# Kernel tuning notes

Measured on AMD Instinct MI355X. Metric: run time of the kernel, lower is better.

The kernel has to match this reference:

```python
import jax, jax.numpy as jnp
import numpy as np

MODEL_DIM = 1024
NUM_HEADS = 16
K_DIM = MODEL_DIM // NUM_HEADS


def setup_inputs() -> dict:
    key = jax.random.key(0)
    k1, k2, k3 = jax.random.split(key, 3)
    x = jax.random.normal(k1, (4, 2048, MODEL_DIM), dtype=jnp.float32)
    # nn.Linear(model_dim, 3*model_dim, bias=False): store as [D, 3D] so y = x @ W
    wqkv = jax.random.normal(k2, (MODEL_DIM, 3 * MODEL_DIM), dtype=jnp.float32) * (MODEL_DIM ** -0.5)
    wo = jax.random.normal(k3, (MODEL_DIM, MODEL_DIM), dtype=jnp.float32) * (MODEL_DIM ** -0.5)
    return {"x": x, "wqkv": wqkv, "wo": wo}


def reference(x, wqkv, wo):
    B, L, D = x.shape
    H, K = NUM_HEADS, K_DIM
    qkv = jnp.einsum("bld,de->ble", x, wqkv)  # [B, L, 3D]
    q, k, v = jnp.split(qkv, 3, axis=-1)
    # Faithful to source: plain reshape (no transpose) into [B, H, L, K]
    qh = q.reshape(B, H, L, K)
    kh = k.reshape(B, H, L, K)
    vh = v.reshape(B, H, L, K)
    scores = jnp.einsum("bhlk,bhmk->bhlm", qh, kh) / jnp.sqrt(jnp.float32(K))
    # Faithful quirk: softmax over dim=1 (head axis), as in the source
    probs = jax.nn.softmax(scores, axis=1)
    attended = jnp.einsum("bhlm,bhmk->bhlk", probs, vh)  # [B, H, L, K]
    concatted = attended.transpose(0, 2, 1, 3).reshape(B, L, D)
    return jnp.einsum("bld,de->ble", concatted, wo)
```

## Files before the change

### kernel.cpp

```cpp
#include <hip/hip_runtime.h>
#include <hip/hip_bf16.h>
#include <stdint.h>

typedef __attribute__((ext_vector_type(8))) short short8;
typedef __attribute__((ext_vector_type(4))) float floatx4;

#define QSCALE 0.18033688f

__device__ __forceinline__ unsigned short f2bf(float f) {
    unsigned int u = __float_as_uint(f);
    u += 0x7fffu + ((u >> 16) & 1u);
    return (unsigned short)(u >> 16);
}
__device__ __forceinline__ unsigned int pack2bf(float a, float b) {
    __hip_bfloat162 h = __float22bfloat162_rn(make_float2(a, b));
    return *reinterpret_cast<unsigned int*>(&h);
}

__device__ __forceinline__ void async16(const void* g, void* l) {
    __builtin_amdgcn_global_load_lds(
        (const __attribute__((address_space(1))) unsigned int*)g,
        (__attribute__((address_space(3))) unsigned int*)l, 16, 0, 0);
}

__global__ __launch_bounds__(256) void cvt_bf16(const float* __restrict__ src,
                                                unsigned short* __restrict__ dst, int n8) {
    int i = blockIdx.x * 256 + threadIdx.x;
    if (i >= n8) return;
    const float4 a = ((const float4*)src)[2 * i];
    const float4 b = ((const float4*)src)[2 * i + 1];
    ushort4 lo, hi;
    lo.x = f2bf(a.x); lo.y = f2bf(a.y); lo.z = f2bf(a.z); lo.w = f2bf(a.w);
    hi.x = f2bf(b.x); hi.y = f2bf(b.y); hi.z = f2bf(b.z); hi.w = f2bf(b.w);
    ((ushort4*)dst)[2 * i] = lo;
    ((ushort4*)dst)[2 * i + 1] = hi;
}

__global__ __launch_bounds__(256) void tcvt(const float* __restrict__ src,
                                            unsigned short* __restrict__ dst, int R, int C) {
    __shared__ unsigned short t[64][72];
    const int tid = threadIdx.x;
    const int r0 = blockIdx.y * 64, c0 = blockIdx.x * 64;
    #pragma unroll
    for (int it = 0; it < 4; it++) {
        int idx = it * 256 + tid;
        int rr = idx >> 4, cc = (idx & 15) * 4;
        float4 v = *(const float4*)(src + (size_t)(r0 + rr) * C + c0 + cc);
        t[cc + 0][rr] = f2bf(v.x);
        t[cc + 1][rr] = f2bf(v.y);
        t[cc + 2][rr] = f2bf(v.z);
        t[cc + 3][rr] = f2bf(v.w);
    }
    __syncthreads();
    #pragma unroll
    for (int it = 0; it < 2; it++) {
        int idx = it * 256 + tid;
        int cc = idx >> 3, r8 = (idx & 7) * 8;
        short8 v = *(const short8*)&t[cc][r8];
        *(short8*)(dst + (size_t)(c0 + cc) * R + r0 + r8) = v;
    }
}

__global__ __launch_bounds__(256) void vtrans(const unsigned short* __restrict__ vb,
                                              unsigned short* __restrict__ vbt) {
    __shared__ unsigned short t[64][72];
    const int tid = threadIdx.x;
    const int bh = blockIdx.y, m0 = blockIdx.x * 64;
    const unsigned short* src = vb + ((size_t)bh * 2048 + m0) * 64;
    unsigned short* dst = vbt + ((size_t)bh << 17) + m0;
    union { short8 v; unsigned short u[8]; } tmp;
    #pragma unroll
    for (int it = 0; it < 2; it++) {
        int idx = it * 256 + tid;
        int m = idx >> 3, c8 = (idx & 7) * 8;
        tmp.v = *(const short8*)(src + (size_t)m * 64 + c8);
        #pragma unroll
        for (int j = 0; j < 8; j++) t[c8 + j][m] = tmp.u[j];
    }
    __syncthreads();
    #pragma unroll
    for (int it = 0; it < 2; it++) {
        int idx = it * 256 + tid;
        int k = idx >> 3, c8 = (idx & 7) * 8;
        short8 v = *(const short8*)&t[k][c8];
        *(short8*)(dst + (size_t)k * 2048 + c8) = v;
    }
}

__global__ __launch_bounds__(256) void qkv_gemm(
    const unsigned short* __restrict__ A, const unsigned short* __restrict__ Bt,
    unsigned short* __restrict__ qb, unsigned short* __restrict__ kb,
    unsigned short* __restrict__ vb)
{
    __shared__ __align__(16) unsigned short Smem[2 * 128 * 32];
    unsigned short* As = Smem;
    unsigned short* Bs = Smem + 128 * 32;
    const int tid = threadIdx.x, wave = tid >> 6, lane = tid & 63;
    const int quad = lane >> 4, lr = lane & 15;
    const int wr = wave >> 1, wc = wave & 1;
    const int bm = blockIdx.y * 128, bn = blockIdx.x * 128;
    const int lrow = lane >> 2, lcol = (lane & 3) * 8;

    floatx4 acc[4][4];
    #pragma unroll
    for (int i = 0; i < 4; i++)
        #pragma unroll
        for (int j = 0; j < 4; j++) acc[i][j] = (floatx4)0.0f;

    for (int k0 = 0; k0 < 1024; k0 += 32) {
        #pragma unroll
        for (int t = 0; t < 2; t++) {
            const int rbase = wave * 32 + t * 16;
            const int r = rbase + lrow;
            async16(A  + (size_t)(bm + r) * 1024 + k0 + lcol, &As[rbase * 32]);
            async16(Bt + (size_t)(bn + r) * 1024 + k0 + lcol, &Bs[rbase * 32]);
        }
        __syncthreads();
        short8 af[4], bfr[4];
        #pragma unroll
        for (int i = 0; i < 4; i++)
            af[i] = *(const short8*)&As[(wr * 64 + i * 16 + lr) * 32 + quad * 8];
        #pragma unroll
        for (int j = 0; j < 4; j++)
            bfr[j] = *(const short8*)&Bs[(wc * 64 + j * 16 + lr) * 32 + quad * 8];
        #pragma unroll
        for (int i = 0; i < 4; i++)
            #pragma unroll
            for (int j = 0; j < 4; j++)
                acc[i][j] = __builtin_amdgcn_mfma_f32_16x16x32_bf16(af[i], bfr[j], acc[i][j], 0, 0, 0);
        __syncthreads();
    }

    const int part = bn >> 10;
    unsigned short* __restrict__ dstb = (part == 0) ? qb : ((part == 1) ? kb : vb);
    const float sc = (part == 0) ? QSCALE : 1.0f;
    const int dblk = ((bn & 1023) >> 6) + wc;
    unsigned short* ep = Smem + wave * 2048;

    #pragma unroll
    for (int half = 0; half < 2; half++) {
        #pragma unroll
        for (int il = 0; il < 2; il++) {
            const int i = half * 2 + il;
            #pragma unroll
            for (int j = 0; j < 4; j++)
                #pragma unroll
                for (int r = 0; r < 4; r++)
                    ep[(il * 16 + quad * 4 + r) * 64 + j * 16 + lr] = f2bf(acc[i][j][r] * sc);
        }
        #pragma unroll
        for (int it = 0; it < 4; it++) {
            const int slot = it * 64 + lane;
            const int rr = slot >> 3, c8 = (slot & 7) * 8;
            short8 v = *(const short8*)&ep[rr * 64 + c8];
            const int row = bm + wr * 64 + half * 32 + rr;
            const int bidx = row >> 11, lseq = row & 2047;
            const int h = lseq >> 7;
            const int l2 = (lseq & 127) * 16 + dblk;
            *(short8*)(dstb + (((size_t)(bidx * 16 + h) * 2048 + l2) << 6) + c8) = v;
        }
    }
}

__global__ __launch_bounds__(256) void out_gemm(
    const unsigned short* __restrict__ A, const unsigned short* __restrict__ Bt,
    float* __restrict__ C)
{
    __shared__ __align__(16) unsigned short As[128 * 32];
    __shared__ __align__(16) unsigned short Bs[128 * 32];
    const int tid = threadIdx.x, wave = tid >> 6, lane = tid & 63;
    const int quad = lane >> 4, lr = lane & 15;
    const int wr = wave >> 1, wc = wave & 1;
    const int bm = blockIdx.y * 128, bn = blockIdx.x * 128;
    const int lrow = lane >> 2, lcol = (lane & 3) * 8;

    floatx4 acc[4][4];
    #pragma unroll
    for (int i = 0; i < 4; i++)
        #pragma unroll
        for (int j = 0; j < 4; j++) acc[i][j] = (floatx4)0.0f;

    for (int k0 = 0; k0 < 1024; k0 += 32) {
        #pragma unroll
        for (int t = 0; t < 2; t++) {
            const int rbase = wave * 32 + t * 16;
            const int r = rbase + lrow;
            async16(A  + (size_t)(bm + r) * 1024 + k0 + lcol, &As[rbase * 32]);
            async16(Bt + (size_t)(bn + r) * 1024 + k0 + lcol, &Bs[rbase * 32]);
        }
        __syncthreads();
        short8 af[4], bfr[4];
        #pragma unroll
        for (int i = 0; i < 4; i++)
            af[i] = *(const short8*)&As[(wr * 64 + i * 16 + lr) * 32 + quad * 8];
        #pragma unroll
        for (int j = 0; j < 4; j++)
            bfr[j] = *(const short8*)&Bs[(wc * 64 + j * 16 + lr) * 32 + quad * 8];
        #pragma unroll
        for (int i = 0; i < 4; i++)
            #pragma unroll
            for (int j = 0; j < 4; j++)
                acc[i][j] = __builtin_amdgcn_mfma_f32_16x16x32_bf16(af[i], bfr[j], acc[i][j], 0, 0, 0);
        __syncthreads();
    }
    #pragma unroll
    for (int i = 0; i < 4; i++)
        #pragma unroll
        for (int j = 0; j < 4; j++)
            #pragma unroll
            for (int r = 0; r < 4; r++) {
                int row = bm + wr * 64 + i * 16 + quad * 4 + r;
                int col = bn + wc * 64 + j * 16 + lr;
                C[(size_t)row * 1024 + col] = acc[i][j][r];
            }
}

__global__ __launch_bounds__(256, 5) void attn_denom(
    const unsigned short* __restrict__ qb, const unsigned short* __restrict__ kb,
    unsigned short* __restrict__ drpT)
{
    __shared__ __align__(16) unsigned short Qs[2][64 * 64];
    __shared__ __align__(16) unsigned short Ks[2][64 * 64];
    const int tid = threadIdx.x, wave = tid >> 6, lane = tid & 63;
    const int quad = lane >> 4, lr = lane & 15;
    const int e7 = lr & 7;
    const int M0 = blockIdx.x * 64, L0 = blockIdx.y * 64, b = blockIdx.z;

    const int klr = lane >> 3;
    const int ksw8 = ((lane & 7) ^ klr) * 8;
    const size_t hb0 = ((size_t)(b * 16)) << 17;
    const unsigned short* qsrc0 = qb + hb0 + (size_t)(L0 + wave * 8 + klr) * 64 + ksw8;
    const unsigned short* ksrc0 = kb + hb0 + (size_t)(M0 + wave * 8 + klr) * 64 + ksw8;

    floatx4 e[4];
    #pragma unroll
    for (int i = 0; i < 4; i++) e[i] = (floatx4)0.0f;

    async16(qsrc0,           &Qs[0][(wave * 8) * 64]);
    async16(qsrc0 + 32 * 64, &Qs[0][(32 + wave * 8) * 64]);
    async16(ksrc0,           &Ks[0][(wave * 8) * 64]);
    async16(ksrc0 + 32 * 64, &Ks[0][(32 + wave * 8) * 64]);
    __syncthreads();

    for (int h = 0; h < 16; h++) {
        const int cur = h & 1, nxt = cur ^ 1;
        if (h < 15) {
            const unsigned short* qs = qsrc0 + ((size_t)(h + 1) << 17);
            const unsigned short* ks = ksrc0 + ((size_t)(h + 1) << 17);
            async16(qs,           &Qs[nxt][(wave * 8) * 64]);
            async16(qs + 32 * 64, &Qs[nxt][(32 + wave * 8) * 64]);
            async16(ks,           &Ks[nxt][(wave * 8) * 64]);
            async16(ks + 32 * 64, &Ks[nxt][(32 + wave * 8) * 64]);
        }
        const unsigned short* qsp = &Qs[cur][0];
        const unsigned short* ksp = &Ks[cur][0];
        const int rq = wave * 16 + lr;
        short8 qf0 = *(const short8*)&qsp[rq * 64 + (quad ^ e7) * 8];
        short8 qf1 = *(const short8*)&qsp[rq * 64 + ((4 + quad) ^ e7) * 8];
        #pragma unroll
        for (int mt = 0; mt < 4; mt++) {
            const int rk = mt * 16 + lr;
            short8 kf0 = *(const short8*)&ksp[rk * 64 + (quad ^ e7) * 8];
            short8 kf1 = *(const short8*)&ksp[rk * 64 + ((4 + quad) ^ e7) * 8];
            floatx4 s = (floatx4)0.0f;
            __builtin_amdgcn_s_setprio(1);
            s = __builtin_amdgcn_mfma_f32_16x16x32_bf16(kf0, qf0, s, 0, 0, 0);
            s = __builtin_amdgcn_mfma_f32_16x16x32_bf16(kf1, qf1, s, 0, 0, 0);
            __builtin_amdgcn_s_setprio(0);
            e[mt][0] += __builtin_amdgcn_exp2f(s[0]);
            e[mt][1] += __builtin_amdgcn_exp2f(s[1]);
            e[mt][2] += __builtin_amdgcn_exp2f(s[2]);
            e[mt][3] += __builtin_amdgcn_exp2f(s[3]);
        }
        if (h < 15) __syncthreads();
    }
    #pragma unroll
    for (int mt = 0; mt < 4; mt++) {
        float r0 = __builtin_amdgcn_rcpf(e[mt][0]);
        float r1 = __builtin_amdgcn_rcpf(e[mt][1]);
        float r2 = __builtin_amdgcn_rcpf(e[mt][2]);
        float r3 = __builtin_amdgcn_rcpf(e[mt][3]);
        uint2 o;
        o.x = pack2bf(r0, r1);
        o.y = pack2bf(r2, r3);
        int mtg = (M0 >> 4) + mt;
        int ltg = (L0 >> 4) + wave;
        *(uint2*)(drpT + ((((size_t)b * 128 + mtg) * 128 + ltg) << 8) + lane * 4) = o;
    }
}

__global__ __launch_bounds__(256, 4) void attn_pv(
    const unsigned short* __restrict__ qb, const unsigned short* __restrict__ kb,
    const unsigned short* __restrict__ vbt, const unsigned short* __restrict__ drpT,
    unsigned short* __restrict__ cb)
{
    __shared__ __align__(16) unsigned short KV[3][64 * 64];
    __shared__ __align__(16) unsigned short Ps[128 * 64];
    const int tid = threadIdx.x, wave = tid >> 6, lane = tid & 63;
    const int quad = lane >> 4, lr = lane & 15;
    const int e7 = lr & 7;
    const int flat = blockIdx.x;
    const int swz = (flat & 7) * 128 + (flat >> 3);
    const int Lt = swz & 15;
    const int h = (swz >> 4) & 15;
    const int b = swz >> 8;
    const int L0 = Lt * 128;
    const size_t head = (size_t)(b * 16 + h);
    const unsigned short* qbase = qb + (head << 17);
    const unsigned short* kbase = kb + (head << 17);
    const unsigned short* vtb   = vbt + (head << 17);
    const unsigned short* dbase = drpT + (((size_t)b * 128 * 128 + (L0 >> 4) + wave * 2) << 8) + lane * 4;

    const int klr = lane >> 3;
    const int ksw = (lane & 7) ^ klr;
    const unsigned short* ksrc0 = kbase + (size_t)(wave * 8 + klr) * 64 + ksw * 8;
    const unsigned short* vsrc0 = vtb + (size_t)(wave * 8 + klr) * 2048 + ksw * 8;

    short8 qf[2][2];
    #pragma unroll
    for (int j = 0; j < 2; j++) {
        const unsigned short* qr = qbase + (size_t)(L0 + wave * 32 + j * 16 + lr) * 64;
        qf[j][0] = *(const short8*)(qr + quad * 8);
        qf[j][1] = *(const short8*)(qr + 32 + quad * 8);
    }

    floatx4 oacc[2][4];
    #pragma unroll
    for (int i = 0; i < 2; i++)
        #pragma unroll
        for (int j = 0; j < 4; j++) oacc[i][j] = (floatx4)0.0f;

    async16(ksrc0,             &KV[0][(wave * 8) * 64]);
    async16(ksrc0 + 32 * 64,   &KV[0][(32 + wave * 8) * 64]);
    async16(vsrc0,             &KV[1][(wave * 8) * 64]);
    async16(vsrc0 + 32 * 2048, &KV[1][(32 + wave * 8) * 64]);
    uint2 du[4][2];
    #pragma unroll
    for (int mt = 0; mt < 4; mt++)
        #pragma unroll
        for (int j = 0; j < 2; j++)
            du[mt][j] = *(const uint2*)(dbase + ((size_t)mt << 15) + (j << 8));
    __syncthreads();

    int kcur = 0, vcur = 1, sp = 2;
    for (int t = 0; t < 32; t++) {
        const int M0 = t * 64;
        if (t < 31) {
            const unsigned short* ks = ksrc0 + (size_t)(M0 + 64) * 64;
            async16(ks,           &KV[sp][(wave * 8) * 64]);
            async16(ks + 32 * 64, &KV[sp][(32 + wave * 8) * 64]);
        }
        const unsigned short* ksp = &KV[kcur][0];
        #pragma unroll
        for (int mt = 0; mt < 4; mt++) {
            const int rk = mt * 16 + lr;
            short8 kf0 = *(const short8*)&ksp[rk * 64 + (quad ^ e7) * 8];
            short8 kf1 = *(const short8*)&ksp[rk * 64 + ((4 + quad) ^ e7) * 8];
            #pragma unroll
            for (int j = 0; j < 2; j++) {
                uint2 duv = du[mt][j];
                floatx4 s = (floatx4)0.0f;
                __builtin_amdgcn_s_setprio(1);
                s = __builtin_amdgcn_mfma_f32_16x16x32_bf16(kf0, qf[j][0], s, 0, 0, 0);
                s = __builtin_amdgcn_mfma_f32_16x16x32_bf16(kf1, qf[j][1], s, 0, 0, 0);
                __builtin_amdgcn_s_setprio(0);
                float r0 = __uint_as_float(duv.x << 16);
                float r1 = __uint_as_float(duv.x & 0xffff0000u);
                float r2 = __uint_as_float(duv.y << 16);
                float r3 = __uint_as_float(duv.y & 0xffff0000u);
                float p0 = __builtin_amdgcn_exp2f(s[0]) * r0;
                float p1 = __builtin_amdgcn_exp2f(s[1]) * r1;
                float p2 = __builtin_amdgcn_exp2f(s[2]) * r2;
                float p3 = __builtin_amdgcn_exp2f(s[3]) * r3;
                uint2 o;
                o.x = pack2bf(p0, p1);
                o.y = pack2bf(p2, p3);
                const int l_loc = wave * 32 + j * 16 + lr;
                const int lb16 = mt * 2 + (quad >> 1);
                *(uint2*)&Ps[l_loc * 64 + (lb16 ^ e7) * 8 + (quad & 1) * 4] = o;
            }
        }
        if (t < 31) {
            __syncthreads();
            const unsigned short* vs = vsrc0 + (M0 + 64);
            async16(vs,             &KV[kcur][(wave * 8) * 64]);
            async16(vs + 32 * 2048, &KV[kcur][(32 + wave * 8) * 64]);
            #pragma unroll
            for (int mt = 0; mt < 4; mt++)
                #pragma unroll
                for (int j = 0; j < 2; j++)
                    du[mt][j] = *(const uint2*)(dbase + (((size_t)((t + 1) * 4 + mt)) << 15) + (j << 8));
        }
        __builtin_amdgcn_sched_barrier(0);
        const unsigned short* vsp = &KV[vcur][0];
        #pragma unroll
        for (int f = 0; f < 2; f++) {
            short8 pf[2], vf[4];
            #pragma unroll
            for (int i2 = 0; i2 < 2; i2++)
                pf[i2] = *(const short8*)&Ps[(wave * 32 + i2 * 16 + lr) * 64 + ((f * 4 + quad) ^ e7) * 8];
            #pragma unroll
            for (int j2 = 0; j2 < 4; j2++) {
                const int rv = j2 * 16 + lr;
                vf[j2] = *(const short8*)&vsp[rv * 64 + ((f * 4 + quad) ^ e7) * 8];
            }
            __builtin_amdgcn_s_setprio(1);
            #pragma unroll
            for (int j2 = 0; j2 < 4; j2++)
                #pragma unroll
                for (int i2 = 0; i2 < 2; i2++)
                    oacc[i2][j2] = __builtin_amdgcn_mfma_f32_16x16x32_bf16(
                        pf[i2], vf[j2], oacc[i2][j2], 0, 0, 0);
            __builtin_amdgcn_s_setprio(0);
        }
        if (t < 31) {
            __syncthreads();
            const int ok = kcur;
            kcur = sp;
            sp = vcur;
            vcur = ok;
        }
    }
    #pragma unroll
    for (int i2 = 0; i2 < 2; i2++)
        #pragma unroll
        for (int j2 = 0; j2 < 4; j2++)
            #pragma unroll
            for (int r = 0; r < 4; r++) {
                int row = L0 + wave * 32 + i2 * 16 + quad * 4 + r;
                int col = h * 64 + j2 * 16 + lr;
                cb[(size_t)(b * 2048 + row) * 1024 + col] = f2bf(oacc[i2][j2][r]);
            }
}

extern "C" void kernel_launch(void* const* d_in, const int* in_sizes, int n_in,
                              void* d_out, int out_size, void* d_ws, size_t ws_size,
                              hipStream_t stream) {
    const float* x    = (const float*)d_in[0];
    const float* wqkv = (const float*)d_in[1];
    const float* wo   = (const float*)d_in[2];
    float* out = (float*)d_out;

    unsigned short* W = (unsigned short*)d_ws;
    unsigned short* qb   = W;
    unsigned short* kb   = W + 8388608;
    unsigned short* vbt  = W + 16777216;
    unsigned short* drpT = W + 25165824;
    unsigned short* cb   = W + 41943040;
    unsigned short* xb    = drpT;
    unsigned short* wqkvT = drpT + 8388608;
    unsigned short* vb    = cb;
    unsigned short* woT   = drpT;

    cvt_bf16  <<<4096, 256, 0, stream>>>(x, xb, 1048576);
    tcvt      <<<dim3(48, 16), 256, 0, stream>>>(wqkv, wqkvT, 1024, 3072);
    qkv_gemm  <<<dim3(24, 64), 256, 0, stream>>>(xb, wqkvT, qb, kb, vb);
    vtrans    <<<dim3(32, 64), 256, 0, stream>>>(vb, vbt);
    attn_denom<<<dim3(32, 32, 4), 256, 0, stream>>>(qb, kb, drpT);
    attn_pv   <<<1024, 256, 0, stream>>>(qb, kb, vbt, drpT, cb);
    tcvt      <<<dim3(16, 16), 256, 0, stream>>>(wo, woT, 1024, 1024);
    out_gemm  <<<dim3(8, 64), 256, 0, stream>>>(cb, woT, out);
}
```

Baseline: 352.6 us.

## Split attn_pv key tile across waves, keep P in registers, reduce partials

attn_pv now gives each wave a 16-key slice of the 64-key tile for a 64-query block, instead of each wave owning 32 query rows. The probabilities stay in registers and feed the PV MFMA as zero-padded half operands, which drops the Ps shared buffer and its LDS round trip. Partial outputs from the four waves are summed through shared memory at the end, and the grid doubles to 2048 blocks with launch bounds relaxed to 3. The trade-off is that half of each PV MFMA's K dimension is padding, the QK work is duplicated across more blocks, and the final reduction needs extra syncs.

```diff
diff --git a/kernel.cpp b/kernel.cpp
--- a/kernel.cpp
+++ b/kernel.cpp
@@ -21,6 +21,17 @@
     __builtin_amdgcn_global_load_lds(
         (const __attribute__((address_space(1))) unsigned int*)g,
         (__attribute__((address_space(3))) unsigned int*)l, 16, 0, 0);
+}
+
+__device__ __forceinline__ short8 padA(uint2 p) {
+    union { uint4 u; short8 s; } t;
+    t.u.x = p.x; t.u.y = p.y; t.u.z = 0u; t.u.w = 0u;
+    return t.s;
+}
+__device__ __forceinline__ short8 dupB(uint2 v) {
+    union { uint4 u; short8 s; } t;
+    t.u.x = v.x; t.u.y = v.y; t.u.z = v.x; t.u.w = v.y;
+    return t.s;
 }
 
 __global__ __launch_bounds__(256) void cvt_bf16(const float* __restrict__ src,
@@ -289,44 +300,43 @@
     }
 }
 
-__global__ __launch_bounds__(256, 4) void attn_pv(
+__global__ __launch_bounds__(256, 3) void attn_pv(
     const unsigned short* __restrict__ qb, const unsigned short* __restrict__ kb,
     const unsigned short* __restrict__ vbt, const unsigned short* __restrict__ drpT,
     unsigned short* __restrict__ cb)
 {
     __shared__ __align__(16) unsigned short KV[3][64 * 64];
-    __shared__ __align__(16) unsigned short Ps[128 * 64];
     const int tid = threadIdx.x, wave = tid >> 6, lane = tid & 63;
     const int quad = lane >> 4, lr = lane & 15;
     const int e7 = lr & 7;
     const int flat = blockIdx.x;
-    const int swz = (flat & 7) * 128 + (flat >> 3);
-    const int Lt = swz & 15;
-    const int h = (swz >> 4) & 15;
-    const int b = swz >> 8;
-    const int L0 = Lt * 128;
+    const int swz = (flat & 7) * 256 + (flat >> 3);
+    const int Lt = swz & 31;
+    const int h = (swz >> 5) & 15;
+    const int b = swz >> 9;
+    const int L0 = Lt * 64;
     const size_t head = (size_t)(b * 16 + h);
     const unsigned short* qbase = qb + (head << 17);
     const unsigned short* kbase = kb + (head << 17);
     const unsigned short* vtb   = vbt + (head << 17);
-    const unsigned short* dbase = drpT + (((size_t)b * 128 * 128 + (L0 >> 4) + wave * 2) << 8) + lane * 4;
+    const unsigned short* dbase = drpT + (((size_t)b * 128 + wave) * 128 + (L0 >> 4)) * 256 + lane * 4;
 
     const int klr = lane >> 3;
     const int ksw = (lane & 7) ^ klr;
     const unsigned short* ksrc0 = kbase + (size_t)(wave * 8 + klr) * 64 + ksw * 8;
     const unsigned short* vsrc0 = vtb + (size_t)(wave * 8 + klr) * 2048 + ksw * 8;
 
-    short8 qf[2][2];
-    #pragma unroll
-    for (int j = 0; j < 2; j++) {
-        const unsigned short* qr = qbase + (size_t)(L0 + wave * 32 + j * 16 + lr) * 64;
-        qf[j][0] = *(const short8*)(qr + quad * 8);
-        qf[j][1] = *(const short8*)(qr + 32 + quad * 8);
-    }
-
-    floatx4 oacc[2][4];
-    #pragma unroll
-    for (int i = 0; i < 2; i++)
+    short8 qf[4][2];
+    #pragma unroll
+    for (int lt = 0; lt < 4; lt++) {
+        const unsigned short* qr = qbase + (size_t)(L0 + lt * 16 + lr) * 64;
+        qf[lt][0] = *(const short8*)(qr + quad * 8);
+        qf[lt][1] = *(const short8*)(qr + 32 + quad * 8);
+    }
+
+    floatx4 oacc[4][4];
+    #pragma unroll
+    for (int i = 0; i < 4; i++)
         #pragma unroll
         for (int j = 0; j < 4; j++) oacc[i][j] = (floatx4)0.0f;
 
@@ -334,13 +344,13 @@
     async16(ksrc0 + 32 * 64,   &KV[0][(32 + wave * 8) * 64]);
     async16(vsrc0,             &KV[1][(wave * 8) * 64]);
     async16(vsrc0 + 32 * 2048, &KV[1][(32 + wave * 8) * 64]);
-    uint2 du[4][2];
-    #pragma unroll
-    for (int mt = 0; mt < 4; mt++)
-        #pragma unroll
-        for (int j = 0; j < 2; j++)
-            du[mt][j] = *(const uint2*)(dbase + ((size_t)mt << 15) + (j << 8));
+    uint2 du[4];
+    #pragma unroll
+    for (int lt = 0; lt < 4; lt++)
+        du[lt] = *(const uint2*)(dbase + (lt << 8));
     __syncthreads();
+
+    const int vblk = (((wave * 2 + (quad >> 1)) ^ e7) << 3) + ((quad & 1) << 2);
 
     int kcur = 0, vcur = 1, sp = 2;
     for (int t = 0; t < 32; t++) {
@@ -351,34 +361,28 @@
             async16(ks + 32 * 64, &KV[sp][(32 + wave * 8) * 64]);
         }
         const unsigned short* ksp = &KV[kcur][0];
-        #pragma unroll
-        for (int mt = 0; mt < 4; mt++) {
-            const int rk = mt * 16 + lr;
-            short8 kf0 = *(const short8*)&ksp[rk * 64 + (quad ^ e7) * 8];
-            short8 kf1 = *(const short8*)&ksp[rk * 64 + ((4 + quad) ^ e7) * 8];
-            #pragma unroll
-            for (int j = 0; j < 2; j++) {
-                uint2 duv = du[mt][j];
-                floatx4 s = (floatx4)0.0f;
-                __builtin_amdgcn_s_setprio(1);
-                s = __builtin_amdgcn_mfma_f32_16x16x32_bf16(kf0, qf[j][0], s, 0, 0, 0);
-                s = __builtin_amdgcn_mfma_f32_16x16x32_bf16(kf1, qf[j][1], s, 0, 0, 0);
-                __builtin_amdgcn_s_setprio(0);
-                float r0 = __uint_as_float(duv.x << 16);
-                float r1 = __uint_as_float(duv.x & 0xffff0000u);
-                float r2 = __uint_as_float(duv.y << 16);
-                float r3 = __uint_as_float(duv.y & 0xffff0000u);
-                float p0 = __builtin_amdgcn_exp2f(s[0]) * r0;
-                float p1 = __builtin_amdgcn_exp2f(s[1]) * r1;
-                float p2 = __builtin_amdgcn_exp2f(s[2]) * r2;
-                float p3 = __builtin_amdgcn_exp2f(s[3]) * r3;
-                uint2 o;
-                o.x = pack2bf(p0, p1);
-                o.y = pack2bf(p2, p3);
-                const int l_loc = wave * 32 + j * 16 + lr;
-                const int lb16 = mt * 2 + (quad >> 1);
-                *(uint2*)&Ps[l_loc * 64 + (lb16 ^ e7) * 8 + (quad & 1) * 4] = o;
-            }
+        const int rk = wave * 16 + lr;
+        short8 kf0 = *(const short8*)&ksp[rk * 64 + (quad ^ e7) * 8];
+        short8 kf1 = *(const short8*)&ksp[rk * 64 + ((4 + quad) ^ e7) * 8];
+        uint2 pa[4];
+        #pragma unroll
+        for (int lt = 0; lt < 4; lt++) {
+            uint2 duv = du[lt];
+            floatx4 s = (floatx4)0.0f;
+            __builtin_amdgcn_s_setprio(1);
+            s = __builtin_amdgcn_mfma_f32_16x16x32_bf16(kf0, qf[lt][0], s, 0, 0, 0);
+            s = __builtin_amdgcn_mfma_f32_16x16x32_bf16(kf1, qf[lt][1], s, 0, 0, 0);
+            __builtin_amdgcn_s_setprio(0);
+            float r0 = __uint_as_float(duv.x << 16);
+            float r1 = __uint_as_float(duv.x & 0xffff0000u);
+            float r2 = __uint_as_float(duv.y << 16);
+            float r3 = __uint_as_float(duv.y & 0xffff0000u);
+            float p0 = __builtin_amdgcn_exp2f(s[0]) * r0;
+            float p1 = __builtin_amdgcn_exp2f(s[1]) * r1;
+            float p2 = __builtin_amdgcn_exp2f(s[2]) * r2;
+            float p3 = __builtin_amdgcn_exp2f(s[3]) * r3;
+            pa[lt].x = pack2bf(p0, p1);
+            pa[lt].y = pack2bf(p2, p3);
         }
         if (t < 31) {
             __syncthreads();
@@ -386,31 +390,20 @@
             async16(vs,             &KV[kcur][(wave * 8) * 64]);
             async16(vs + 32 * 2048, &KV[kcur][(32 + wave * 8) * 64]);
             #pragma unroll
-            for (int mt = 0; mt < 4; mt++)
-                #pragma unroll
-                for (int j = 0; j < 2; j++)
-                    du[mt][j] = *(const uint2*)(dbase + (((size_t)((t + 1) * 4 + mt)) << 15) + (j << 8));
+            for (int lt = 0; lt < 4; lt++)
+                du[lt] = *(const uint2*)(dbase + ((size_t)(t + 1) << 17) + (lt << 8));
         }
         __builtin_amdgcn_sched_barrier(0);
         const unsigned short* vsp = &KV[vcur][0];
         #pragma unroll
-        for (int f = 0; f < 2; f++) {
-            short8 pf[2], vf[4];
-            #pragma unroll
-            for (int i2 = 0; i2 < 2; i2++)
-                pf[i2] = *(const short8*)&Ps[(wave * 32 + i2 * 16 + lr) * 64 + ((f * 4 + quad) ^ e7) * 8];
-            #pragma unroll
-            for (int j2 = 0; j2 < 4; j2++) {
-                const int rv = j2 * 16 + lr;
-                vf[j2] = *(const short8*)&vsp[rv * 64 + ((f * 4 + quad) ^ e7) * 8];
-            }
+        for (int nt = 0; nt < 4; nt++) {
+            uint2 v = *(const uint2*)&vsp[(nt * 16 + lr) * 64 + vblk];
+            short8 vf = dupB(v);
             __builtin_amdgcn_s_setprio(1);
             #pragma unroll
-            for (int j2 = 0; j2 < 4; j2++)
-                #pragma unroll
-                for (int i2 = 0; i2 < 2; i2++)
-                    oacc[i2][j2] = __builtin_amdgcn_mfma_f32_16x16x32_bf16(
-                        pf[i2], vf[j2], oacc[i2][j2], 0, 0, 0);
+            for (int lt = 0; lt < 4; lt++)
+                oacc[lt][nt] = __builtin_amdgcn_mfma_f32_16x16x32_bf16(
+                    padA(pa[lt]), vf, oacc[lt][nt], 0, 0, 0);
             __builtin_amdgcn_s_setprio(0);
         }
         if (t < 31) {
@@ -421,16 +414,26 @@
             vcur = ok;
         }
     }
-    #pragma unroll
-    for (int i2 = 0; i2 < 2; i2++)
-        #pragma unroll
-        for (int j2 = 0; j2 < 4; j2++)
-            #pragma unroll
-            for (int r = 0; r < 4; r++) {
-                int row = L0 + wave * 32 + i2 * 16 + quad * 4 + r;
-                int col = h * 64 + j2 * 16 + lr;
-                cb[(size_t)(b * 2048 + row) * 1024 + col] = f2bf(oacc[i2][j2][r]);
-            }
+
+    __syncthreads();
+    float* red = (float*)&KV[0][0];
+    #pragma unroll
+    for (int lt = 0; lt < 4; lt++) {
+        #pragma unroll
+        for (int nt = 0; nt < 4; nt++)
+            #pragma unroll
+            for (int r = 0; r < 4; r++)
+                red[(wave * 16 + quad * 4 + r) * 64 + nt * 16 + lr] = oacc[lt][nt][r];
+        __syncthreads();
+        #pragma unroll
+        for (int rr = 0; rr < 4; rr++) {
+            const int row = wave * 4 + rr;
+            float s4 = red[(0 * 16 + row) * 64 + lane] + red[(1 * 16 + row) * 64 + lane]
+                     + red[(2 * 16 + row) * 64 + lane] + red[(3 * 16 + row) * 64 + lane];
+            cb[(size_t)(b * 2048 + L0 + lt * 16 + row) * 1024 + h * 64 + lane] = f2bf(s4);
+        }
+        __syncthreads();
+    }
 }
 
 extern "C" void kernel_launch(void* const* d_in, const int* in_sizes, int n_in,
@@ -457,7 +460,7 @@
     qkv_gemm  <<<dim3(24, 64), 256, 0, stream>>>(xb, wqkvT, qb, kb, vb);
     vtrans    <<<dim3(32, 64), 256, 0, stream>>>(vb, vbt);
     attn_denom<<<dim3(32, 32, 4), 256, 0, stream>>>(qb, kb, drpT);
-    attn_pv   <<<1024, 256, 0, stream>>>(qb, kb, vbt, drpT, cb);
+    attn_pv   <<<2048, 256, 0, stream>>>(qb, kb, vbt, drpT, cb);
     tcvt      <<<dim3(16, 16), 256, 0, stream>>>(wo, woT, 1024, 1024);
     out_gemm  <<<dim3(8, 64), 256, 0, stream>>>(cb, woT, out);
 }
```

After: 389.2 us. 1.1x slower.
